# Optimization experiments

Hardware: AMD Instinct MI355X
Metric: run time of the kernel (lower is better)

Reference implementation:

```python
import jax, jax.numpy as jnp
import numpy as np

B, T, N, F_IN, H, EV = 2, 12, 20000, 9, 64, 9
E = 200000


def setup_inputs() -> dict:
    key = jax.random.key(0)
    k = jax.random.split(key, 24)
    s = 0.1
    rn = lambda kk, shp: s * jax.random.normal(kk, shp, dtype=jnp.float32)
    d = {
        'graph_at_instance': jax.random.normal(k[0], (B, T, N, F_IN), dtype=jnp.float32),
        'target_event': jax.random.normal(k[1], (B, EV), dtype=jnp.float32),
        'input_event': jax.random.normal(k[2], (B, EV), dtype=jnp.float32),
        'edge_weight': jax.random.uniform(k[3], (E,), dtype=jnp.float32),
        'edge_src': jax.random.randint(k[4], (E,), 0, N, dtype=jnp.int32),
        'edge_dst': jax.random.randint(k[5], (E,), 0, N, dtype=jnp.int32),
        # 12 per-timestep GraphSAGE blocks (conv1: 9->64, conv2: 64->64, conv3: 64->9)
        'W1l': rn(k[6], (T, F_IN, H)), 'b1': jnp.zeros((T, H), jnp.float32), 'W1r': rn(k[7], (T, F_IN, H)),
        'W2l': rn(k[8], (T, H, H)),    'b2': jnp.zeros((T, H), jnp.float32), 'W2r': rn(k[9], (T, H, H)),
        'W3l': rn(k[10], (T, H, F_IN)),'b3': jnp.zeros((T, F_IN), jnp.float32), 'W3r': rn(k[11], (T, H, F_IN)),
        # 12 per-timestep GRU cells (9 -> 9), standard GRUCell parameterization
        'Wih': rn(k[12], (T, F_IN, 3 * F_IN)), 'Whh': rn(k[13], (T, F_IN, 3 * F_IN)),
        'bih': jnp.zeros((T, 3 * F_IN), jnp.float32), 'bhh': jnp.zeros((T, 3 * F_IN), jnp.float32),
        # encoder (18 -> 64) and decoder (64 -> 1)
        'enc_W': rn(k[14], (F_IN + EV, 64)), 'enc_b': jnp.zeros((64,), jnp.float32),
        'dec_W': rn(k[15], (64, 1)), 'dec_b': jnp.zeros((1,), jnp.float32),
    }
    return d


def _forward(graph_at_instance, target_event, input_event, edge_weight,
             W1l, b1, W1r, W2l, b2, W2r, W3l, b3, W3r,
             Wih, Whh, bih, bhh, enc_W, enc_b, dec_W, dec_b,
             edge_src, edge_dst):
    # in-degree for mean aggregation (clamped to avoid div by 0)
    deg = jnp.zeros((N,), jnp.float32).at[edge_dst].add(1.0)
    deg = jnp.maximum(deg, 1.0)[None, :, None]  # [1, N, 1]

    def sage(x, Wl, bl, Wr):
        # x: [B, N, d].  Weighted mean aggregation over edges, then lin_l(agg) + lin_r(x).
        m = x[:, edge_src] * edge_weight[None, :, None]          # [B, E, d]
        agg = jnp.zeros_like(x).at[:, edge_dst].add(m) / deg     # [B, N, d]
        return agg @ Wl + bl + x @ Wr

    def gru_cell(x, h, wih, whh, bih_t, bhh_t):
        gi = x @ wih + bih_t
        gh = h @ whh + bhh_t
        gir, giz, gin = jnp.split(gi, 3, axis=-1)
        ghr, ghz, ghn = jnp.split(gh, 3, axis=-1)
        r = jax.nn.sigmoid(gir + ghr)
        z = jax.nn.sigmoid(giz + ghz)
        n = jnp.tanh(gin + r * ghn)
        return (1.0 - z) * n + z * h

    def step(h, xs):
        xt, w1l, bb1, w1r, w2l, bb2, w2r, w3l, bb3, w3r, wih, whh, bih_t, bhh_t = xs
        x = jax.nn.elu(sage(xt, w1l, bb1, w1r))
        x = jax.nn.elu(sage(x, w2l, bb2, w2r))
        x = jax.nn.elu(sage(x, w3l, bb3, w3r))
        h = gru_cell(x, h, wih, whh, bih_t, bhh_t)
        return h, h

    xs = (jnp.swapaxes(graph_at_instance, 0, 1),  # [T, B, N, 9]
          W1l, b1, W1r, W2l, b2, W2r, W3l, b3, W3r, Wih, Whh, bih, bhh)
    h0 = jnp.zeros((B, N, F_IN), jnp.float32)
    _, outs = jax.lax.scan(step, h0, xs)          # [T, B, N, 9]
    outs = jnp.swapaxes(outs, 0, 1)               # [B, T, N, 9]

    te = jnp.broadcast_to(target_event[:, None, None, :], (B, T, N, EV))
    x = jnp.concatenate([outs, te], axis=-1)      # [B, T, N, 18]
    out = (x @ enc_W + enc_b) @ dec_W + dec_b     # [B, T, N, 1]
    mask = (graph_at_instance[..., 0:1] != 0).astype(out.dtype)
    return out * mask


def reference(graph_at_instance, target_event, input_event, edge_weight,
              W1l, b1, W1r, W2l, b2, W2r, W3l, b3, W3r,
              Wih, Whh, bih, bhh, enc_W, enc_b, dec_W, dec_b,
              edge_src, edge_dst):
    return _forward(graph_at_instance, target_event, input_event, edge_weight,
                    W1l, b1, W1r, W2l, b2, W2r, W3l, b3, W3r,
                    Wih, Whh, bih, bhh, enc_W, enc_b, dec_W, dec_b,
                    edge_src, edge_dst)
```

## Files before the change

kernel.cpp:

```cpp
#include <hip/hip_runtime.h>
#include <hip/hip_bf16.h>

#define BB 2
#define TT 12
#define NN 20000
#define FF 9
#define HH 64
#define EE 200000

typedef __hip_bfloat16 bf;
typedef __attribute__((ext_vector_type(8))) short s8v;
typedef __attribute__((ext_vector_type(4))) float f4v;

__device__ unsigned g_xa[TT*NN*HH];
__device__ unsigned g_ag[TT*NN*HH];
__device__ unsigned g_xb[TT*NN*HH];
__device__ float2   g_x9[TT*NN*FF];
__device__ float2   g_xp[TT*NN*FF];
__device__ float2   g_z9[TT*NN*FF];
__device__ float2   g_r9[TT*NN*FF];
__device__ int      g_rp[NN+1];
__device__ int      g_cnt[NN];
__device__ int      g_csrc[EE];
__device__ float    g_cw[EE];
__device__ float    g_cvec[32];

__device__ __forceinline__ float lo2f(unsigned u){ unsigned v=u<<16; float f; __builtin_memcpy(&f,&v,4); return f; }
__device__ __forceinline__ float hi2f(unsigned u){ unsigned v=u&0xffff0000u; float f; __builtin_memcpy(&f,&v,4); return f; }
__device__ __forceinline__ unsigned short f2us(float f){ bf h=__float2bfloat16(f); unsigned short u; __builtin_memcpy(&u,&h,2); return u; }
__device__ __forceinline__ unsigned pack2(float a0, float a1){ return (unsigned)f2us(a0) | ((unsigned)f2us(a1)<<16); }
__device__ __forceinline__ float elu(float x){ return x>0.f ? x : expm1f(x); }
__device__ __forceinline__ float rdl(float v, int l){
  int i; __builtin_memcpy(&i,&v,4);
  int r = __builtin_amdgcn_readlane(i, l);
  float f; __builtin_memcpy(&f,&r,4);
  return f;
}

__global__ void k_zero(){
  int i = blockIdx.x*256 + threadIdx.x;
  if(i < NN) g_cnt[i] = 0;
}
__global__ void k_count(const int* __restrict__ dst){
  int e = blockIdx.x*256 + threadIdx.x;
  if(e < EE) atomicAdd(&g_cnt[dst[e]], 1);
}
__global__ void k_scan(){
  __shared__ int part[256];
  const int CH = 79;
  int t = threadIdx.x;
  int base = t*CH;
  int s = 0;
  for(int i=0;i<CH;i++){ int idx=base+i; if(idx<NN) s += g_cnt[idx]; }
  part[t] = s; __syncthreads();
  for(int off=1; off<256; off<<=1){
    int v = (t>=off) ? part[t-off] : 0;
    __syncthreads();
    part[t] += v;
    __syncthreads();
  }
  int run = (t==0) ? 0 : part[t-1];
  for(int i=0;i<CH;i++){
    int idx=base+i;
    if(idx<NN){ run += g_cnt[idx]; g_rp[idx+1] = run; }
  }
  if(t==0) g_rp[0] = 0;
}
__global__ void k_fill(const int* __restrict__ dst, const int* __restrict__ src,
                       const float* __restrict__ ew){
  int e = blockIdx.x*256 + threadIdx.x;
  if(e >= EE) return;
  int d = dst[e];
  int pos = g_rp[d] + atomicAdd(&g_cnt[d], 1);
  g_csrc[pos] = src[e];
  g_cw[pos]   = ew[e];
}

__global__ void k_head(const float* __restrict__ encW, const float* __restrict__ encb,
                       const float* __restrict__ decW, const float* __restrict__ decb,
                       const float* __restrict__ te){
  __shared__ float c[19];
  int tid = threadIdx.x;
  if(tid < 18){ float s=0.f; for(int j=0;j<64;j++) s += encW[tid*64+j]*decW[j]; c[tid]=s; }
  if(tid == 18){ float s=decb[0]; for(int j=0;j<64;j++) s += encb[j]*decW[j]; c[18]=s; }
  __syncthreads();
  if(tid < FF) g_cvec[tid] = c[tid];
  if(tid < BB){ float s=c[18]; for(int k=0;k<FF;k++) s += te[tid*FF+k]*c[9+k]; g_cvec[FF+tid]=s; }
}

__global__ void k_pack(const float* __restrict__ g){
  long i = (long)blockIdx.x*256 + threadIdx.x;
  if(i < (long)TT*NN*FF){
    float2 p;
    p.x = g[i];
    p.y = g[(long)TT*NN*FF + i];
    g_xp[i] = p;
  }
}

__global__ void k_conv1_all(const float* __restrict__ Wl, const float* __restrict__ bias,
                            const float* __restrict__ Wr){
  int t = blockIdx.y;
  int tid = threadIdx.x;
  int lane = tid & 63;
  int grp  = lane >> 4;
  int sub  = lane & 15;
  bool act = sub < FF;
  float wl[FF], wr[FF];
  #pragma unroll
  for(int f=0; f<FF; f++){
    wl[f] = Wl[(size_t)t*FF*HH + f*HH + lane];
    wr[f] = Wr[(size_t)t*FF*HH + f*HH + lane];
  }
  float breg = bias[t*HH + lane];
  int wid = (blockIdx.x*256+tid)>>6, nw = gridDim.x*4;
  const float2* __restrict__ xp = g_xp + (size_t)t*NN*FF;
  size_t tb = (size_t)t*NN;
  for(int n=wid; n<NN; n+=nw){
    int r0=g_rp[n], r1=g_rp[n+1];
    float dg = fmaxf((float)(r1-r0), 1.f);
    float inv = 1.f/dg;
    float2 agg = {0.f, 0.f};
    for(int base=r0; base<r1; base+=64){
      int cnt = min(64, r1-base);
      int ms = 0; float mw = 0.f;
      if(lane < cnt){ ms = g_csrc[base+lane]; mw = g_cw[base+lane]; }
      for(int k=0;k<cnt;k+=4){
        int   sg = __shfl(ms, k+grp, 64);
        float wg = __shfl(mw, k+grp, 64);
        if(act){
          float2 v = xp[(size_t)sg*FF + sub];
          agg.x += wg*v.x;
          agg.y += wg*v.y;
        }
      }
    }
    agg.x += __shfl_xor(agg.x,16,64); agg.y += __shfl_xor(agg.y,16,64);
    agg.x += __shfl_xor(agg.x,32,64); agg.y += __shfl_xor(agg.y,32,64);
    agg.x *= inv; agg.y *= inv;
    float2 xv = {0.f,0.f};
    if(lane < FF) xv = xp[(size_t)n*FF + lane];
    float a0 = breg, a1 = breg;
    #pragma unroll
    for(int f=0; f<FF; f++){
      float ax=rdl(agg.x,f), ay=rdl(agg.y,f);
      float sx=rdl(xv.x,f),  sy=rdl(xv.y,f);
      a0 += ax*wl[f] + sx*wr[f];
      a1 += ay*wl[f] + sy*wr[f];
    }
    g_xa[(tb+n)*HH+lane] = pack2(elu(a0), elu(a1));
  }
}

__global__ void k_agg_all(){
  const unsigned* __restrict__ src = g_xa;
  int tid = threadIdx.x;
  int lane = tid & 63;
  int grp  = lane >> 4;
  int sub  = lane & 15;
  int wid = (blockIdx.x*256+tid)>>6, nw = gridDim.x*4;
  for(int idx=wid; idx<TT*NN; idx+=nw){
    unsigned ut = (unsigned)idx / NN;
    int n = idx - (int)(ut*NN);
    size_t tb = (size_t)ut*NN;
    const unsigned* __restrict__ rowp = src + tb*HH + (sub<<2);
    int r0=g_rp[n], r1=g_rp[n+1];
    float dg = fmaxf((float)(r1-r0), 1.f);
    float inv = 1.f/dg;
    float p0[4]={0.f,0.f,0.f,0.f}, p1[4]={0.f,0.f,0.f,0.f};
    for(int base=r0; base<r1; base+=64){
      int cnt = min(64, r1-base);
      int ms = 0; float mw = 0.f;
      if(lane < cnt){ ms = g_csrc[base+lane]; mw = g_cw[base+lane]; }
      for(int k=0;k<cnt;k+=4){
        int   sg = __shfl(ms, k+grp, 64);
        float wg = __shfl(mw, k+grp, 64);
        const uint4 v = *reinterpret_cast<const uint4*>(rowp + (size_t)sg*HH);
        p0[0]+=wg*lo2f(v.x); p1[0]+=wg*hi2f(v.x);
        p0[1]+=wg*lo2f(v.y); p1[1]+=wg*hi2f(v.y);
        p0[2]+=wg*lo2f(v.z); p1[2]+=wg*hi2f(v.z);
        p0[3]+=wg*lo2f(v.w); p1[3]+=wg*hi2f(v.w);
      }
    }
    #pragma unroll
    for(int q=0;q<4;q++){
      p0[q] += __shfl_xor(p0[q],16,64); p1[q] += __shfl_xor(p1[q],16,64);
      p0[q] += __shfl_xor(p0[q],32,64); p1[q] += __shfl_xor(p1[q],32,64);
    }
    if(lane < 16){
      uint4 o;
      o.x = pack2(p0[0]*inv, p1[0]*inv);
      o.y = pack2(p0[1]*inv, p1[1]*inv);
      o.z = pack2(p0[2]*inv, p1[2]*inv);
      o.w = pack2(p0[3]*inv, p1[3]*inv);
      *reinterpret_cast<uint4*>(g_ag + (tb + (size_t)n)*HH + (lane<<2)) = o;
    }
  }
}

__global__ __launch_bounds__(256) void k_gemm2_all(const float* __restrict__ Wl,
                                                   const float* __restrict__ bias,
                                                   const float* __restrict__ Wr){
  int t = blockIdx.y;
  __shared__ float sW[128*65];
  int tid = threadIdx.x;
  for(int i=tid; i<64*64; i+=256){
    int r = i >> 6, c = i & 63;
    sW[r*65+c]      = Wl[(size_t)t*4096 + i];
    sW[(r+64)*65+c] = Wr[(size_t)t*4096 + i];
  }
  __syncthreads();
  int lane = tid & 63, wave = tid >> 6;
  int quad = lane >> 4, col = lane & 15;
  int base16 = blockIdx.x*64 + wave*16;
  if(base16 >= NN) return;
  size_t tb = (size_t)t*NN;
  int nodeA = base16 + col;
  s8v A0[4], A1[4];
  #pragma unroll
  for(int ks=0; ks<4; ks++){
    const unsigned* srcb = (ks < 2) ? g_ag : g_xa;
    int koff = (ks & 1)*32 + quad*8;
    const uint4 u = *reinterpret_cast<const uint4*>(srcb + (tb+nodeA)*HH + koff);
    const uint4 v = *reinterpret_cast<const uint4*>(srcb + (tb+nodeA)*HH + koff + 4);
    unsigned uu[8] = {u.x,u.y,u.z,u.w,v.x,v.y,v.z,v.w};
    #pragma unroll
    for(int j=0;j<8;j++){
      A0[ks][j] = (short)(uu[j] & 0xffffu);
      A1[ks][j] = (short)(uu[j] >> 16);
    }
  }
  #pragma unroll
  for(int nt=0; nt<4; nt++){
    f4v c0 = {0.f,0.f,0.f,0.f}, c1 = {0.f,0.f,0.f,0.f};
    #pragma unroll
    for(int ks=0; ks<4; ks++){
      s8v B;
      #pragma unroll
      for(int j=0;j<8;j++)
        B[j] = (short)f2us(sW[(ks*32+quad*8+j)*65 + nt*16+col]);
      c0 = __builtin_amdgcn_mfma_f32_16x16x32_bf16(A0[ks], B, c0, 0, 0, 0);
      c1 = __builtin_amdgcn_mfma_f32_16x16x32_bf16(A1[ks], B, c1, 0, 0, 0);
    }
    float bn = bias[t*HH + nt*16 + col];
    #pragma unroll
    for(int reg=0; reg<4; reg++){
      int node = base16 + quad*4 + reg;
      g_xb[(tb+node)*HH + nt*16 + col] = pack2(elu(c0[reg]+bn), elu(c1[reg]+bn));
    }
  }
}

__global__ __launch_bounds__(256) void k_gemm3z(const float* __restrict__ Wl,
                                                const float* __restrict__ bias,
                                                const float* __restrict__ Wr){
  int t = blockIdx.y;
  __shared__ float sW[128*10];
  int tid = threadIdx.x;
  for(int i=tid; i<64*FF; i+=256){
    int r = i/FF, c = i - r*FF;
    sW[r*10+c]      = Wl[(size_t)t*HH*FF + i];
    sW[(r+64)*10+c] = Wr[(size_t)t*HH*FF + i];
  }
  __syncthreads();
  int lane = tid & 63, wave = tid >> 6;
  int quad = lane >> 4, col = lane & 15;
  int base16 = blockIdx.x*64 + wave*16;
  if(base16 >= NN) return;
  size_t tb = (size_t)t*NN;
  int nodeA = base16 + col;
  f4v z0={0.f,0.f,0.f,0.f}, z1={0.f,0.f,0.f,0.f};
  f4v r0={0.f,0.f,0.f,0.f}, r1={0.f,0.f,0.f,0.f};
  #pragma unroll
  for(int ks=0; ks<2; ks++){
    int koff = ks*32 + quad*8;
    const uint4 u = *reinterpret_cast<const uint4*>(g_xb + (tb+nodeA)*HH + koff);
    const uint4 v = *reinterpret_cast<const uint4*>(g_xb + (tb+nodeA)*HH + koff + 4);
    unsigned uu[8] = {u.x,u.y,u.z,u.w,v.x,v.y,v.z,v.w};
    s8v A0, A1, Bl, Br;
    #pragma unroll
    for(int j=0;j<8;j++){
      A0[j] = (short)(uu[j] & 0xffffu);
      A1[j] = (short)(uu[j] >> 16);
      int row = ks*32 + quad*8 + j;
      Bl[j] = (col < FF) ? (short)f2us(sW[row*10 + col])      : (short)0;
      Br[j] = (col < FF) ? (short)f2us(sW[(row+64)*10 + col]) : (short)0;
    }
    z0 = __builtin_amdgcn_mfma_f32_16x16x32_bf16(A0, Bl, z0, 0, 0, 0);
    z1 = __builtin_amdgcn_mfma_f32_16x16x32_bf16(A1, Bl, z1, 0, 0, 0);
    r0 = __builtin_amdgcn_mfma_f32_16x16x32_bf16(A0, Br, r0, 0, 0, 0);
    r1 = __builtin_amdgcn_mfma_f32_16x16x32_bf16(A1, Br, r1, 0, 0, 0);
  }
  if(col < FF){
    float bn = bias[t*FF + col];
    #pragma unroll
    for(int reg=0; reg<4; reg++){
      int node = base16 + quad*4 + reg;
      float2 oz; oz.x = z0[reg]; oz.y = z1[reg];
      float2 orr; orr.x = r0[reg]+bn; orr.y = r1[reg]+bn;
      g_z9[(tb+node)*FF + col] = oz;
      g_r9[(tb+node)*FF + col] = orr;
    }
  }
}

__global__ void k_agg9f(){
  int t = blockIdx.y;
  int tid = threadIdx.x;
  int lane = tid & 63;
  int grp  = lane >> 4;
  int sub  = lane & 15;
  bool act = sub < FF;
  int wid = (blockIdx.x*256+tid)>>6, nw = gridDim.x*4;
  const float2* __restrict__ zp = g_z9 + (size_t)t*NN*FF;
  size_t tb = (size_t)t*NN;
  for(int n=wid; n<NN; n+=nw){
    int r0=g_rp[n], r1=g_rp[n+1];
    float dg = fmaxf((float)(r1-r0), 1.f);
    float inv = 1.f/dg;
    float2 agg = {0.f, 0.f};
    for(int base=r0; base<r1; base+=64){
      int cnt = min(64, r1-base);
      int ms = 0; float mw = 0.f;
      if(lane < cnt){ ms = g_csrc[base+lane]; mw = g_cw[base+lane]; }
      for(int k=0;k<cnt;k+=4){
        int   sg = __shfl(ms, k+grp, 64);
        float wg = __shfl(mw, k+grp, 64);
        if(act){
          float2 v = zp[(size_t)sg*FF + sub];
          agg.x += wg*v.x;
          agg.y += wg*v.y;
        }
      }
    }
    agg.x += __shfl_xor(agg.x,16,64); agg.y += __shfl_xor(agg.y,16,64);
    agg.x += __shfl_xor(agg.x,32,64); agg.y += __shfl_xor(agg.y,32,64);
    if(lane < FF){
      float2 r = g_r9[(tb+n)*FF + lane];
      float2 o;
      o.x = elu(agg.x*inv + r.x);
      o.y = elu(agg.y*inv + r.y);
      g_x9[(tb+n)*FF + lane] = o;
    }
  }
}

__global__ __launch_bounds__(256) void k_gru_fused(const float* __restrict__ g,
                          const float* __restrict__ Wih, const float* __restrict__ Whh,
                          const float* __restrict__ bih, const float* __restrict__ bhh,
                          float* __restrict__ out){
  __shared__ float sWih[TT*FF*27];
  __shared__ float sWhh[TT*FF*27];
  __shared__ float sbih[TT*27], sbhh[TT*27];
  int tid = threadIdx.x;
  for(int i=tid;i<TT*FF*27;i+=256){ sWih[i]=Wih[i]; sWhh[i]=Whh[i]; }
  for(int i=tid;i<TT*27;i+=256){ sbih[i]=bih[i]; sbhh[i]=bhh[i]; }
  __syncthreads();
  int lane = tid & 63;
  int wv   = tid >> 6;
  int p    = lane / 9;
  int f    = lane - p*9;
  int gbase = p*9;
  int id = (blockIdx.x*4 + wv)*7 + p;
  bool valid = (p < 7) && (id < BB*NN);
  int b = 0, n = 0;
  if(valid){ b = (id >= NN) ? 1 : 0; n = id - b*NN; }
  float c9[FF];
  #pragma unroll
  for(int i=0;i<FF;i++) c9[i] = g_cvec[i];
  float cb = g_cvec[FF+b];
  float h = 0.f;
  float hs[FF];
  #pragma unroll
  for(int i=0;i<FF;i++) hs[i] = 0.f;
  for(int t=0;t<TT;t++){
    float x = 0.f;
    if(valid){
      float2 xf = g_x9[((size_t)t*NN+n)*FF+f];
      x = b ? xf.y : xf.x;
    }
    float xs[FF];
    #pragma unroll
    for(int i=0;i<FF;i++) xs[i] = __shfl(x, gbase+i, 64);
    const float* wi = &sWih[t*FF*27];
    const float* wh = &sWhh[t*FF*27];
    float gir = sbih[t*27+f], giz = sbih[t*27+9+f], gin = sbih[t*27+18+f];
    float ghr = sbhh[t*27+f], ghz = sbhh[t*27+9+f], ghn = sbhh[t*27+18+f];
    #pragma unroll
    for(int i=0;i<FF;i++){
      float xi = xs[i], hi = hs[i];
      gir += xi*wi[i*27+f];    giz += xi*wi[i*27+9+f];    gin += xi*wi[i*27+18+f];
      ghr += hi*wh[i*27+f];    ghz += hi*wh[i*27+9+f];    ghn += hi*wh[i*27+18+f];
    }
    float r = 1.f/(1.f+__expf(-(gir+ghr)));
    float z = 1.f/(1.f+__expf(-(giz+ghz)));
    float nv = tanhf(gin + r*ghn);
    h = (1.f-z)*nv + z*h;
    #pragma unroll
    for(int i=0;i<FF;i++) hs[i] = __shfl(h, gbase+i, 64);
    if(valid && f == 0){
      float acc = cb;
      #pragma unroll
      for(int i=0;i<FF;i++) acc += hs[i]*c9[i];
      size_t gidx = (size_t)(b*TT+t)*NN + n;
      float m = (g[gidx*FF] != 0.f) ? 1.f : 0.f;
      out[gidx] = acc*m;
    }
  }
}

extern "C" void kernel_launch(void* const* d_in, const int* in_sizes, int n_in,
                              void* d_out, int out_size, void* d_ws, size_t ws_size,
                              hipStream_t stream){
  const float* g    = (const float*)d_in[0];
  const float* te   = (const float*)d_in[1];
  const float* ew   = (const float*)d_in[3];
  const int* esrc = (const int*)d_in[4];
  const int* edst = (const int*)d_in[5];
  const float* W1l=(const float*)d_in[6];  const float* b1 =(const float*)d_in[7];  const float* W1r=(const float*)d_in[8];
  const float* W2l=(const float*)d_in[9];  const float* b2 =(const float*)d_in[10]; const float* W2r=(const float*)d_in[11];
  const float* W3l=(const float*)d_in[12]; const float* b3 =(const float*)d_in[13]; const float* W3r=(const float*)d_in[14];
  const float* Wih=(const float*)d_in[15]; const float* Whh=(const float*)d_in[16];
  const float* bih=(const float*)d_in[17]; const float* bhh=(const float*)d_in[18];
  const float* encW=(const float*)d_in[19]; const float* encb=(const float*)d_in[20];
  const float* decW=(const float*)d_in[21]; const float* decb=(const float*)d_in[22];
  float* out = (float*)d_out;

  k_zero <<<(NN+255)/256, 256, 0, stream>>>();
  k_count<<<(EE+255)/256, 256, 0, stream>>>(edst);
  k_scan <<<1, 256, 0, stream>>>();
  k_zero <<<(NN+255)/256, 256, 0, stream>>>();
  k_fill <<<(EE+255)/256, 256, 0, stream>>>(edst, esrc, ew);
  k_head <<<1, 64, 0, stream>>>(encW, encb, decW, decb, te);
  k_pack <<<((long)TT*NN*FF+255)/256, 256, 0, stream>>>(g);

  dim3 gcv(512, TT);
  dim3 ggm((NN+63)/64, TT);
  k_conv1_all<<<gcv, 256, 0, stream>>>(W1l, b1, W1r);
  k_agg_all<<<2048, 256, 0, stream>>>();
  k_gemm2_all<<<ggm, 256, 0, stream>>>(W2l, b2, W2r);
  k_gemm3z<<<ggm, 256, 0, stream>>>(W3l, b3, W3r);
  k_agg9f<<<gcv, 256, 0, stream>>>();
  int nblk = (BB*NN + 27) / 28;
  k_gru_fused<<<nblk, 256, 0, stream>>>(g, Wih, Whh, bih, bhh, out);
}
```

Before: 581.6 us.

## Split conv1 into aggregation kernel and MFMA bf16 GEMM kernel

The conv1 kernel, which did edge aggregation and then a scalar 18x64 readlane-based matmul per node, is split into two kernels. The first writes the normalized 9-wide aggregate to a new fp32 buffer. The second does the linear layer with bf16 MFMA 16x16x32 tiles, using weights staged in shared memory, and applies bias and ELU. This moves the per-node scalar FMA and readlane work onto matrix cores. In exchange it adds an extra global round-trip for the aggregate, an extra launch, and bf16 rounding of the conv1 inputs and weights.

New measurement: 591.3 us. No clear change (+1.7%).

```diff
diff --git a/kernel.cpp b/kernel.cpp
--- a/kernel.cpp
+++ b/kernel.cpp
@@ -19,6 +19,7 @@
 __device__ float2   g_xp[TT*NN*FF];
 __device__ float2   g_z9[TT*NN*FF];
 __device__ float2   g_r9[TT*NN*FF];
+__device__ float2   g_a9[TT*NN*FF];
 __device__ int      g_rp[NN+1];
 __device__ int      g_cnt[NN];
 __device__ int      g_csrc[EE];
@@ -30,12 +31,6 @@
 __device__ __forceinline__ unsigned short f2us(float f){ bf h=__float2bfloat16(f); unsigned short u; __builtin_memcpy(&u,&h,2); return u; }
 __device__ __forceinline__ unsigned pack2(float a0, float a1){ return (unsigned)f2us(a0) | ((unsigned)f2us(a1)<<16); }
 __device__ __forceinline__ float elu(float x){ return x>0.f ? x : expm1f(x); }
-__device__ __forceinline__ float rdl(float v, int l){
-  int i; __builtin_memcpy(&i,&v,4);
-  int r = __builtin_amdgcn_readlane(i, l);
-  float f; __builtin_memcpy(&f,&r,4);
-  return f;
-}
 
 __global__ void k_zero(){
   int i = blockIdx.x*256 + threadIdx.x;
@@ -98,21 +93,13 @@
   }
 }
 
-__global__ void k_conv1_all(const float* __restrict__ Wl, const float* __restrict__ bias,
-                            const float* __restrict__ Wr){
+__global__ void k_agg1(){
   int t = blockIdx.y;
   int tid = threadIdx.x;
   int lane = tid & 63;
   int grp  = lane >> 4;
   int sub  = lane & 15;
   bool act = sub < FF;
-  float wl[FF], wr[FF];
-  #pragma unroll
-  for(int f=0; f<FF; f++){
-    wl[f] = Wl[(size_t)t*FF*HH + f*HH + lane];
-    wr[f] = Wr[(size_t)t*FF*HH + f*HH + lane];
-  }
-  float breg = bias[t*HH + lane];
   int wid = (blockIdx.x*256+tid)>>6, nw = gridDim.x*4;
   const float2* __restrict__ xp = g_xp + (size_t)t*NN*FF;
   size_t tb = (size_t)t*NN;
@@ -137,18 +124,58 @@
     }
     agg.x += __shfl_xor(agg.x,16,64); agg.y += __shfl_xor(agg.y,16,64);
     agg.x += __shfl_xor(agg.x,32,64); agg.y += __shfl_xor(agg.y,32,64);
-    agg.x *= inv; agg.y *= inv;
-    float2 xv = {0.f,0.f};
-    if(lane < FF) xv = xp[(size_t)n*FF + lane];
-    float a0 = breg, a1 = breg;
-    #pragma unroll
-    for(int f=0; f<FF; f++){
-      float ax=rdl(agg.x,f), ay=rdl(agg.y,f);
-      float sx=rdl(xv.x,f),  sy=rdl(xv.y,f);
-      a0 += ax*wl[f] + sx*wr[f];
-      a1 += ay*wl[f] + sy*wr[f];
-    }
-    g_xa[(tb+n)*HH+lane] = pack2(elu(a0), elu(a1));
+    if(lane < FF){
+      float2 o; o.x = agg.x*inv; o.y = agg.y*inv;
+      g_a9[(tb+n)*FF + lane] = o;
+    }
+  }
+}
+
+__global__ __launch_bounds__(256) void k_gemm1(const float* __restrict__ Wl,
+                                               const float* __restrict__ bias,
+                                               const float* __restrict__ Wr){
+  int t = blockIdx.y;
+  __shared__ float sW[32*65];
+  int tid = threadIdx.x;
+  for(int i=tid; i<32*64; i+=256){
+    int r = i >> 6, c = i & 63;
+    float v = 0.f;
+    if(r < FF)        v = Wl[(size_t)t*FF*HH + r*HH + c];
+    else if(r < 2*FF) v = Wr[(size_t)t*FF*HH + (r-FF)*HH + c];
+    sW[r*65+c] = v;
+  }
+  __syncthreads();
+  int lane = tid & 63, wave = tid >> 6;
+  int quad = lane >> 4, col = lane & 15;
+  int base16 = blockIdx.x*64 + wave*16;
+  if(base16 >= NN) return;
+  size_t tb = (size_t)t*NN;
+  int node = base16 + col;
+  s8v A0, A1;
+  #pragma unroll
+  for(int j=0;j<8;j++){
+    int k = quad*8 + j;
+    float2 v = {0.f, 0.f};
+    if(k < FF)        v = g_a9[(tb+node)*FF + k];
+    else if(k < 2*FF) v = g_xp[(tb+node)*FF + (k-FF)];
+    A0[j] = (short)f2us(v.x);
+    A1[j] = (short)f2us(v.y);
+  }
+  #pragma unroll
+  for(int nt=0; nt<4; nt++){
+    f4v c0 = {0.f,0.f,0.f,0.f}, c1 = {0.f,0.f,0.f,0.f};
+    s8v B;
+    #pragma unroll
+    for(int j=0;j<8;j++)
+      B[j] = (short)f2us(sW[(quad*8+j)*65 + nt*16+col]);
+    c0 = __builtin_amdgcn_mfma_f32_16x16x32_bf16(A0, B, c0, 0, 0, 0);
+    c1 = __builtin_amdgcn_mfma_f32_16x16x32_bf16(A1, B, c1, 0, 0, 0);
+    float bn = bias[t*HH + nt*16 + col];
+    #pragma unroll
+    for(int reg=0; reg<4; reg++){
+      int nd = base16 + quad*4 + reg;
+      g_xa[(tb+nd)*HH + nt*16 + col] = pack2(elu(c0[reg]+bn), elu(c1[reg]+bn));
+    }
   }
 }
 
@@ -436,7 +463,8 @@
 
   dim3 gcv(512, TT);
   dim3 ggm((NN+63)/64, TT);
-  k_conv1_all<<<gcv, 256, 0, stream>>>(W1l, b1, W1r);
+  k_agg1<<<gcv, 256, 0, stream>>>();
+  k_gemm1<<<ggm, 256, 0, stream>>>(W1l, b1, W1r);
   k_agg_all<<<2048, 256, 0, stream>>>();
   k_gemm2_all<<<ggm, 256, 0, stream>>>(W2l, b2, W2r);
   k_gemm3z<<<ggm, 256, 0, stream>>>(W3l, b3, W3r);
```
